# Optimization experiments

Measured on AMD Instinct MI355X. Metric: run time of the kernel, lower is better.

Reference implementation:

```python
import jax, jax.numpy as jnp
import numpy as np

N, E = 50000, 800000
IN, OUT = 128, 64
NEG_SLOPE = 0.2


def setup_inputs() -> dict:
    key = jax.random.key(0)
    ks = jax.random.split(key, 8)
    x = jax.random.normal(ks[0], (N, IN), dtype=jnp.float32)
    edge_index = jax.random.randint(ks[1], (2, E), 0, N, dtype=jnp.int64)
    s_in = 1.0 / np.sqrt(IN)
    s_out = 1.0 / np.sqrt(OUT)
    Wl = jax.random.normal(ks[2], (OUT, IN), dtype=jnp.float32) * s_in   # lin_l weight
    bl = jax.random.normal(ks[3], (OUT,), dtype=jnp.float32) * s_in     # lin_l bias
    Wr = jax.random.normal(ks[4], (OUT, IN), dtype=jnp.float32) * s_in  # lin_r weight
    br = jax.random.normal(ks[5], (OUT,), dtype=jnp.float32) * s_in     # lin_r bias
    att = jax.random.normal(ks[6], (OUT,), dtype=jnp.float32) * s_out   # attention vector a
    bias = jnp.zeros((OUT,), dtype=jnp.float32)                          # final output bias
    return dict(x=x, Wl=Wl, bl=bl, Wr=Wr, br=br, att=att, bias=bias, edge_index=edge_index)


def reference(x, Wl, bl, Wr, br, att, bias, edge_index):
    n = x.shape[0]
    loop = jnp.arange(n, dtype=edge_index.dtype)
    src = jnp.concatenate([edge_index[0], loop])  # add_self_loops=True
    dst = jnp.concatenate([edge_index[1], loop])
    xl = x @ Wl.T + bl  # [N, OUT] source transform (x_j)
    xr = x @ Wr.T + br  # [N, OUT] target transform (x_i)
    h = xl[src] + xr[dst]                              # [E+N, OUT]
    h = jnp.where(h > 0, h, NEG_SLOPE * h)             # LeakyReLU(0.2)
    e = h @ att                                        # [E+N] edge logits
    # segment softmax over destination nodes (every node has a self-loop)
    m = jax.ops.segment_max(e, dst, num_segments=n)
    ex = jnp.exp(e - m[dst])
    s = jax.ops.segment_sum(ex, dst, num_segments=n)
    alpha = ex / s[dst]
    out = jax.ops.segment_sum(alpha[:, None] * xl[src], dst, num_segments=n) + bias
    return jax.nn.relu(out)  # norm=Identity, dropout inactive at inference
```

## Files before the change

### kernel.cpp

```cpp
#include <hip/hip_runtime.h>
#include <hip/hip_bf16.h>

#define NEG_SLOPE 0.2f
#define CAP 5120
#define CHUNK 4096
#define LOG2E 1.4426950408889634f

typedef __attribute__((ext_vector_type(8))) short short8v;
typedef __attribute__((ext_vector_type(4))) short short4v;
typedef __attribute__((ext_vector_type(4))) float f32x4;

__device__ __forceinline__ short f2bf(float f) {
  __hip_bfloat16 b = __float2bfloat16(f);
  return *reinterpret_cast<short*>(&b);
}
__device__ __forceinline__ float bf2f(short s) {
  return __uint_as_float(((unsigned)(unsigned short)s) << 16);
}

__device__ __forceinline__ float row_reduce16(float p) {
  p += __int_as_float(__builtin_amdgcn_update_dpp(
      0, __float_as_int(p), 0xB1, 0xF, 0xF, true));
  p += __int_as_float(__builtin_amdgcn_update_dpp(
      0, __float_as_int(p), 0x4E, 0xF, 0xF, true));
  p += __int_as_float(__builtin_amdgcn_update_dpp(
      0, __float_as_int(p), 0x124, 0xF, 0xF, true));
  p += __int_as_float(__builtin_amdgcn_update_dpp(
      0, __float_as_int(p), 0x128, 0xF, 0xF, true));
  return p;
}

__global__ __launch_bounds__(256) void k_prep(
    const float* __restrict__ Wl, const float* __restrict__ Wr,
    const float* __restrict__ bl, const float* __restrict__ br,
    short* __restrict__ W2, float* __restrict__ biasc,
    int* __restrict__ bcur, int nbk) {
  int idx = blockIdx.x * 256 + threadIdx.x;
  if (idx < 128 * 128) {
    int j = idx >> 7, k = idx & 127;
    float v = (j < 64) ? Wl[j * 128 + k] : Wr[(j - 64) * 128 + k];
    W2[idx] = f2bf(v);
  } else {
    int z = idx - 128 * 128;
    if (z < nbk) bcur[z] = 0;
  }
  if (idx < 128) biasc[idx] = (idx < 64) ? bl[idx] : br[idx - 64];
}

__global__ __launch_bounds__(256) void k_tbf(
    const float* __restrict__ x, const short* __restrict__ W2,
    const float* __restrict__ biasc, const int* __restrict__ eidx,
    int* __restrict__ bcur, unsigned* __restrict__ pk,
    short* __restrict__ xlb, float* __restrict__ xr, int nN, int E_,
    int nbf) {
  __shared__ union {
    struct { int hist[256]; int base[256]; } bf;
    short xs[64 * 136];
  } u;
  const int t = threadIdx.x;

  if (blockIdx.x < nbf) {
    u.bf.hist[t] = 0;
    __syncthreads();
    const int e0 = blockIdx.x * CHUNK + t * 16;
    unsigned mypk[16];
    int myrank[16];
    const bool valid = (e0 < E_);
    if (valid) {
      const int4* ps = (const int4*)(eidx + e0);
      const int4* pd = (const int4*)(eidx + E_ + e0);
#pragma unroll
      for (int j = 0; j < 4; ++j) {
        int4 sv = ps[j];
        int4 dv = pd[j];
        int ss[4] = {sv.x, sv.y, sv.z, sv.w};
        int dd[4] = {dv.x, dv.y, dv.z, dv.w};
#pragma unroll
        for (int q = 0; q < 4; ++q) {
          unsigned p = ((unsigned)dd[q] << 16) | (unsigned)ss[q];
          mypk[j * 4 + q] = p;
          myrank[j * 4 + q] = atomicAdd(&u.bf.hist[dd[q] >> 8], 1);
        }
      }
    }
    __syncthreads();
    u.bf.base[t] = u.bf.hist[t] ? atomicAdd(&bcur[t], u.bf.hist[t]) : 0;
    __syncthreads();
    if (valid) {
#pragma unroll
      for (int j = 0; j < 16; ++j) {
        int b = mypk[j] >> 24;
        unsigned idx = (unsigned)(u.bf.base[b] + myrank[j]);
        if (idx < CAP) pk[(unsigned)b * CAP + idx] = mypk[j];
      }
    }
    return;
  }

  const int n0 = (blockIdx.x - nbf) * 64;
#pragma unroll
  for (int i = 0; i < 8; ++i) {
    int f = (i * 256 + t) * 4;
    int node = f >> 7, k = f & 127;
    int gn = min(n0 + node, nN - 1);
    float4 v = *(const float4*)(x + (size_t)gn * 128 + k);
    short4v s4;
    s4[0] = f2bf(v.x); s4[1] = f2bf(v.y); s4[2] = f2bf(v.z); s4[3] = f2bf(v.w);
    *(short4v*)(u.xs + node * 136 + k) = s4;
  }
  __syncthreads();

  const int w = t >> 6;
  const int lane = t & 63;
  const int r = lane & 15;
  const int kb = lane >> 4;

  short8v bfr[2][4];
#pragma unroll
  for (int c = 0; c < 2; ++c) {
    const short* bp = W2 + (size_t)((w * 2 + c) * 16 + r) * 128 + kb * 8;
#pragma unroll
    for (int kk = 0; kk < 4; ++kk) bfr[c][kk] = *(const short8v*)(bp + kk * 32);
  }

  f32x4 acc[4][2];
#pragma unroll
  for (int nt = 0; nt < 4; ++nt)
#pragma unroll
    for (int c = 0; c < 2; ++c) acc[nt][c] = (f32x4){0.f, 0.f, 0.f, 0.f};

#pragma unroll
  for (int nt = 0; nt < 4; ++nt) {
    short8v afr[4];
#pragma unroll
    for (int kk = 0; kk < 4; ++kk)
      afr[kk] =
          *(const short8v*)(u.xs + (nt * 16 + r) * 136 + kb * 8 + kk * 32);
#pragma unroll
    for (int kk = 0; kk < 4; ++kk) {
      acc[nt][0] =
          __builtin_amdgcn_mfma_f32_16x16x32_bf16(afr[kk], bfr[0][kk],
                                                  acc[nt][0], 0, 0, 0);
      acc[nt][1] =
          __builtin_amdgcn_mfma_f32_16x16x32_bf16(afr[kk], bfr[1][kk],
                                                  acc[nt][1], 0, 0, 0);
    }
  }

#pragma unroll
  for (int c = 0; c < 2; ++c) {
    const int ch = (w * 2 + c) * 16 + r;
    const float bv = biasc[ch];
#pragma unroll
    for (int nt = 0; nt < 4; ++nt) {
#pragma unroll
      for (int i = 0; i < 4; ++i) {
        int node = n0 + nt * 16 + kb * 4 + i;
        if (node < nN) {
          float v = acc[nt][c][i] + bv;
          if (ch < 64) xlb[(size_t)node * 64 + ch] = f2bf(v);
          else         xr[(size_t)node * 64 + (ch - 64)] = v;
        }
      }
    }
  }
}

__global__ __launch_bounds__(256) void k_nfill(
    const unsigned* __restrict__ pk, const int* __restrict__ bcur,
    int* __restrict__ rowlo, int* __restrict__ rowhi,
    unsigned short* __restrict__ csr, int nN) {
  __shared__ int hist[256];
  __shared__ int nbase[256];
  __shared__ int wsum[4];
  const int b = blockIdx.x;
  const int t = threadIdx.x;
  const int nb0 = b << 8;
  const int cnt = min(bcur[b], CAP);
  const unsigned gbase = (unsigned)b * CAP;
  hist[t] = 0;
  __syncthreads();
  for (int i = t; i < cnt; i += 256)
    atomicAdd(&hist[(pk[gbase + i] >> 16) & 255], 1);
  __syncthreads();
  const int lane = t & 63;
  const int wid = t >> 6;
  int v = hist[t];
  const int orig = v;
#pragma unroll
  for (int off = 1; off < 64; off <<= 1) {
    int uu = __shfl_up(v, off);
    if (lane >= off) v += uu;
  }
  if (lane == 63) wsum[wid] = v;
  __syncthreads();
  int add = 0;
  for (int ww = 0; ww < wid; ++ww) add += wsum[ww];
  const int excl = v - orig + add;
  nbase[t] = excl;
  if (nb0 + t < nN) {
    rowlo[nb0 + t] = (int)gbase + excl;
    rowhi[nb0 + t] = (int)gbase + excl + orig;
  }
  __syncthreads();
  hist[t] = 0;
  __syncthreads();
  for (int i = t; i < cnt; i += 256) {
    unsigned p = pk[gbase + i];
    int dl = (p >> 16) & 255;
    int slot = nbase[dl] + atomicAdd(&hist[dl], 1);
    csr[gbase + slot] = (unsigned short)(p & 0xFFFFu);
  }
}

__global__ __launch_bounds__(256) void k_node(
    const int* __restrict__ rowlo, const int* __restrict__ rowhi,
    const unsigned short* __restrict__ csr, const short* __restrict__ xlb,
    const float* __restrict__ xr, const float* __restrict__ att,
    const float* __restrict__ bias, float* __restrict__ out, int nN) {
  const int wid = (blockIdx.x * 256 + threadIdx.x) >> 6;
  if (wid >= nN) return;
  const int lane = threadIdx.x & 63;
  const int g = lane >> 4;
  const int r = lane & 15;
  const int d = wid;

  const float4 att4 = ((const float4*)att)[r];
  const float4 xr4 = *(const float4*)(xr + (size_t)d * 64 + r * 4);

  short4v sb = *(const short4v*)(xlb + (size_t)d * 64 + r * 4);
  float4 xls = make_float4(bf2f(sb[0]), bf2f(sb[1]), bf2f(sb[2]), bf2f(sb[3]));

  float hh, ps = 0.f;
  hh = xls.x + xr4.x; hh = fmaxf(hh, NEG_SLOPE * hh); ps = fmaf(hh, att4.x, ps);
  hh = xls.y + xr4.y; hh = fmaxf(hh, NEG_SLOPE * hh); ps = fmaf(hh, att4.y, ps);
  hh = xls.z + xr4.z; hh = fmaxf(hh, NEG_SLOPE * hh); ps = fmaf(hh, att4.z, ps);
  hh = xls.w + xr4.w; hh = fmaxf(hh, NEG_SLOPE * hh); ps = fmaf(hh, att4.w, ps);
  ps = row_reduce16(ps) * LOG2E;

  const bool g0 = (g == 0);
  float m = ps;
  float ssum = g0 ? 1.f : 0.f;
  float4 acc = g0 ? xls : make_float4(0.f, 0.f, 0.f, 0.f);

  const int lo = rowlo[d], hi = rowhi[d];
  const int nst = (hi - lo + 3) >> 2;

#define PROC(VREG, SIDX)                                                      \
  {                                                                           \
    const bool act = ((SIDX) < hi);                                           \
    float4 xlv = make_float4(bf2f(VREG[0]), bf2f(VREG[1]), bf2f(VREG[2]),     \
                             bf2f(VREG[3]));                                  \
    float p = 0.f;                                                            \
    hh = xlv.x + xr4.x; hh = fmaxf(hh, NEG_SLOPE * hh);                       \
    p = fmaf(hh, att4.x, p);                                                  \
    hh = xlv.y + xr4.y; hh = fmaxf(hh, NEG_SLOPE * hh);                       \
    p = fmaf(hh, att4.y, p);                                                  \
    hh = xlv.z + xr4.z; hh = fmaxf(hh, NEG_SLOPE * hh);                       \
    p = fmaf(hh, att4.z, p);                                                  \
    hh = xlv.w + xr4.w; hh = fmaxf(hh, NEG_SLOPE * hh);                       \
    p = fmaf(hh, att4.w, p);                                                  \
    p = row_reduce16(p);                                                      \
    const float pm = act ? p * LOG2E : -3.0e38f;                              \
    const float nm = fmaxf(m, pm);                                            \
    const float sc = exp2f(m - nm);                                           \
    const float w = exp2f(pm - nm);                                           \
    ssum = fmaf(ssum, sc, w);                                                 \
    acc.x = fmaf(acc.x, sc, w * xlv.x);                                       \
    acc.y = fmaf(acc.y, sc, w * xlv.y);                                       \
    acc.z = fmaf(acc.z, sc, w * xlv.z);                                       \
    acc.w = fmaf(acc.w, sc, w * xlv.w);                                       \
    m = nm;                                                                   \
  }

  int sA = lo + g, sB = sA + 4, sC = sA + 8, sD = sA + 12;
  short4v vA, vB, vC, vD;
  {
    int srcA = (sA < hi) ? (int)csr[sA] : d;
    vA = *(const short4v*)(xlb + (size_t)srcA * 64 + r * 4);
    int srcB = (sB < hi) ? (int)csr[sB] : d;
    vB = *(const short4v*)(xlb + (size_t)srcB * 64 + r * 4);
    int srcC = (sC < hi) ? (int)csr[sC] : d;
    vC = *(const short4v*)(xlb + (size_t)srcC * 64 + r * 4);
    int srcD = (sD < hi) ? (int)csr[sD] : d;
    vD = *(const short4v*)(xlb + (size_t)srcD * 64 + r * 4);
  }

  int tt = 0;
  for (; tt + 3 < nst; tt += 4) {
    PROC(vA, sA);
    if (tt + 4 < nst) {
      int sN = sA + 16;
      int srcN = (sN < hi) ? (int)csr[sN] : d;
      vA = *(const short4v*)(xlb + (size_t)srcN * 64 + r * 4);
    }
    PROC(vB, sB);
    if (tt + 5 < nst) {
      int sN = sB + 16;
      int srcN = (sN < hi) ? (int)csr[sN] : d;
      vB = *(const short4v*)(xlb + (size_t)srcN * 64 + r * 4);
    }
    PROC(vC, sC);
    if (tt + 6 < nst) {
      int sN = sC + 16;
      int srcN = (sN < hi) ? (int)csr[sN] : d;
      vC = *(const short4v*)(xlb + (size_t)srcN * 64 + r * 4);
    }
    PROC(vD, sD);
    if (tt + 7 < nst) {
      int sN = sD + 16;
      int srcN = (sN < hi) ? (int)csr[sN] : d;
      vD = *(const short4v*)(xlb + (size_t)srcN * 64 + r * 4);
    }
    sA += 16; sB += 16; sC += 16; sD += 16;
  }
  {
    const int rem = nst - tt;
    if (rem > 0) PROC(vA, sA);
    if (rem > 1) PROC(vB, sB);
    if (rem > 2) PROC(vC, sC);
  }
#undef PROC

#pragma unroll
  for (int off = 16; off <= 32; off <<= 1) {
    float mo = __shfl_xor(m, off);
    float so = __shfl_xor(ssum, off);
    float ax = __shfl_xor(acc.x, off);
    float ay = __shfl_xor(acc.y, off);
    float az = __shfl_xor(acc.z, off);
    float aw = __shfl_xor(acc.w, off);
    float nm = fmaxf(m, mo);
    float sa = exp2f(m - nm);
    float sb2 = exp2f(mo - nm);
    ssum = ssum * sa + so * sb2;
    acc.x = acc.x * sa + ax * sb2;
    acc.y = acc.y * sa + ay * sb2;
    acc.z = acc.z * sa + az * sb2;
    acc.w = acc.w * sa + aw * sb2;
    m = nm;
  }

  if (g == 0) {
    const float inv = 1.0f / ssum;
    const float4 b4 = ((const float4*)bias)[r];
    float4 o;
    o.x = fmaxf(fmaf(acc.x, inv, b4.x), 0.f);
    o.y = fmaxf(fmaf(acc.y, inv, b4.y), 0.f);
    o.z = fmaxf(fmaf(acc.z, inv, b4.z), 0.f);
    o.w = fmaxf(fmaf(acc.w, inv, b4.w), 0.f);
    *(float4*)(out + (size_t)d * 64 + r * 4) = o;
  }
}

extern "C" void kernel_launch(void* const* d_in, const int* in_sizes, int n_in,
                              void* d_out, int out_size, void* d_ws,
                              size_t ws_size, hipStream_t stream) {
  const float* x    = (const float*)d_in[0];
  const float* Wl   = (const float*)d_in[1];
  const float* bl   = (const float*)d_in[2];
  const float* Wr   = (const float*)d_in[3];
  const float* br   = (const float*)d_in[4];
  const float* att  = (const float*)d_in[5];
  const float* bias = (const float*)d_in[6];
  const int* eidx   = (const int*)d_in[7];
  float* out = (float*)d_out;

  const int N = in_sizes[0] / 128;
  const int E = in_sizes[7] / 2;
  const int NB = (N + 255) >> 8;
  const int nbf = (E + CHUNK - 1) / CHUNK;
  const int ntr = (N + 63) / 64;

  short* xlb   = (short*)d_ws;
  float* xr    = (float*)(xlb + (size_t)N * 64);
  unsigned* pk = (unsigned*)(xr + (size_t)N * 64);
  unsigned short* csr = (unsigned short*)(pk + (size_t)NB * CAP);
  short* W2    = (short*)(csr + (size_t)NB * CAP);
  float* biasc = (float*)(W2 + 128 * 128);
  int* bcur    = (int*)(biasc + 128);
  int* rowlo   = bcur + NB;
  int* rowhi   = rowlo + N;

  k_prep<<<(128 * 128 + NB + 255) / 256, 256, 0, stream>>>(
      Wl, Wr, bl, br, W2, biasc, bcur, NB);
  k_tbf<<<nbf + ntr, 256, 0, stream>>>(x, W2, biasc, eidx, bcur, pk, xlb, xr,
                                       N, E, nbf);
  k_nfill<<<NB, 256, 0, stream>>>(pk, bcur, rowlo, rowhi, csr, N);
  k_node<<<(N + 3) / 4, 256, 0, stream>>>(rowlo, rowhi, csr, xlb, xr, att,
                                          bias, out, N);
}
```

Before: 82.06 us.

## Split each wave into eight 8-lane edge groups and skip redundant softmax rescales

Result: faster. 78.09 us (-4.8%).

```diff
diff --git a/kernel.cpp b/kernel.cpp
--- a/kernel.cpp
+++ b/kernel.cpp
@@ -18,15 +18,13 @@
   return __uint_as_float(((unsigned)(unsigned short)s) << 16);
 }
 
-__device__ __forceinline__ float row_reduce16(float p) {
+__device__ __forceinline__ float row_reduce8(float p) {
   p += __int_as_float(__builtin_amdgcn_update_dpp(
       0, __float_as_int(p), 0xB1, 0xF, 0xF, true));
   p += __int_as_float(__builtin_amdgcn_update_dpp(
       0, __float_as_int(p), 0x4E, 0xF, 0xF, true));
   p += __int_as_float(__builtin_amdgcn_update_dpp(
-      0, __float_as_int(p), 0x124, 0xF, 0xF, true));
-  p += __int_as_float(__builtin_amdgcn_update_dpp(
-      0, __float_as_int(p), 0x128, 0xF, 0xF, true));
+      0, __float_as_int(p), 0x141, 0xF, 0xF, true));
   return p;
 }
 
@@ -221,135 +219,156 @@
   const int wid = (blockIdx.x * 256 + threadIdx.x) >> 6;
   if (wid >= nN) return;
   const int lane = threadIdx.x & 63;
-  const int g = lane >> 4;
-  const int r = lane & 15;
+  const int g = lane >> 3;
+  const int r = lane & 7;
   const int d = wid;
 
-  const float4 att4 = ((const float4*)att)[r];
-  const float4 xr4 = *(const float4*)(xr + (size_t)d * 64 + r * 4);
-
-  short4v sb = *(const short4v*)(xlb + (size_t)d * 64 + r * 4);
-  float4 xls = make_float4(bf2f(sb[0]), bf2f(sb[1]), bf2f(sb[2]), bf2f(sb[3]));
+  const float4 atA = *(const float4*)(att + r * 8);
+  const float4 atB = *(const float4*)(att + r * 8 + 4);
+  const float4 xrA = *(const float4*)(xr + (size_t)d * 64 + r * 8);
+  const float4 xrB = *(const float4*)(xr + (size_t)d * 64 + r * 8 + 4);
+
+  short8v sv = *(const short8v*)(xlb + (size_t)d * 64 + r * 8);
+  const float s0 = bf2f(sv[0]), s1 = bf2f(sv[1]), s2 = bf2f(sv[2]),
+              s3 = bf2f(sv[3]), s4 = bf2f(sv[4]), s5 = bf2f(sv[5]),
+              s6 = bf2f(sv[6]), s7 = bf2f(sv[7]);
 
   float hh, ps = 0.f;
-  hh = xls.x + xr4.x; hh = fmaxf(hh, NEG_SLOPE * hh); ps = fmaf(hh, att4.x, ps);
-  hh = xls.y + xr4.y; hh = fmaxf(hh, NEG_SLOPE * hh); ps = fmaf(hh, att4.y, ps);
-  hh = xls.z + xr4.z; hh = fmaxf(hh, NEG_SLOPE * hh); ps = fmaf(hh, att4.z, ps);
-  hh = xls.w + xr4.w; hh = fmaxf(hh, NEG_SLOPE * hh); ps = fmaf(hh, att4.w, ps);
-  ps = row_reduce16(ps) * LOG2E;
+  hh = s0 + xrA.x; hh = fmaxf(hh, NEG_SLOPE * hh); ps = fmaf(hh, atA.x, ps);
+  hh = s1 + xrA.y; hh = fmaxf(hh, NEG_SLOPE * hh); ps = fmaf(hh, atA.y, ps);
+  hh = s2 + xrA.z; hh = fmaxf(hh, NEG_SLOPE * hh); ps = fmaf(hh, atA.z, ps);
+  hh = s3 + xrA.w; hh = fmaxf(hh, NEG_SLOPE * hh); ps = fmaf(hh, atA.w, ps);
+  hh = s4 + xrB.x; hh = fmaxf(hh, NEG_SLOPE * hh); ps = fmaf(hh, atB.x, ps);
+  hh = s5 + xrB.y; hh = fmaxf(hh, NEG_SLOPE * hh); ps = fmaf(hh, atB.y, ps);
+  hh = s6 + xrB.z; hh = fmaxf(hh, NEG_SLOPE * hh); ps = fmaf(hh, atB.z, ps);
+  hh = s7 + xrB.w; hh = fmaxf(hh, NEG_SLOPE * hh); ps = fmaf(hh, atB.w, ps);
+  ps = row_reduce8(ps) * LOG2E;
 
   const bool g0 = (g == 0);
   float m = ps;
   float ssum = g0 ? 1.f : 0.f;
-  float4 acc = g0 ? xls : make_float4(0.f, 0.f, 0.f, 0.f);
+  float4 accA = g0 ? make_float4(s0, s1, s2, s3) : make_float4(0, 0, 0, 0);
+  float4 accB = g0 ? make_float4(s4, s5, s6, s7) : make_float4(0, 0, 0, 0);
 
   const int lo = rowlo[d], hi = rowhi[d];
-  const int nst = (hi - lo + 3) >> 2;
+  const int nst = (hi - lo + 7) >> 3;
 
 #define PROC(VREG, SIDX)                                                      \
   {                                                                           \
     const bool act = ((SIDX) < hi);                                           \
-    float4 xlv = make_float4(bf2f(VREG[0]), bf2f(VREG[1]), bf2f(VREG[2]),     \
-                             bf2f(VREG[3]));                                  \
+    const float f0 = bf2f(VREG[0]), f1 = bf2f(VREG[1]), f2 = bf2f(VREG[2]),   \
+                f3 = bf2f(VREG[3]), f4 = bf2f(VREG[4]), f5 = bf2f(VREG[5]),   \
+                f6 = bf2f(VREG[6]), f7 = bf2f(VREG[7]);                       \
     float p = 0.f;                                                            \
-    hh = xlv.x + xr4.x; hh = fmaxf(hh, NEG_SLOPE * hh);                       \
-    p = fmaf(hh, att4.x, p);                                                  \
-    hh = xlv.y + xr4.y; hh = fmaxf(hh, NEG_SLOPE * hh);                       \
-    p = fmaf(hh, att4.y, p);                                                  \
-    hh = xlv.z + xr4.z; hh = fmaxf(hh, NEG_SLOPE * hh);                       \
-    p = fmaf(hh, att4.z, p);                                                  \
-    hh = xlv.w + xr4.w; hh = fmaxf(hh, NEG_SLOPE * hh);                       \
-    p = fmaf(hh, att4.w, p);                                                  \
-    p = row_reduce16(p);                                                      \
+    hh = f0 + xrA.x; hh = fmaxf(hh, NEG_SLOPE * hh); p = fmaf(hh, atA.x, p);  \
+    hh = f1 + xrA.y; hh = fmaxf(hh, NEG_SLOPE * hh); p = fmaf(hh, atA.y, p);  \
+    hh = f2 + xrA.z; hh = fmaxf(hh, NEG_SLOPE * hh); p = fmaf(hh, atA.z, p);  \
+    hh = f3 + xrA.w; hh = fmaxf(hh, NEG_SLOPE * hh); p = fmaf(hh, atA.w, p);  \
+    hh = f4 + xrB.x; hh = fmaxf(hh, NEG_SLOPE * hh); p = fmaf(hh, atB.x, p);  \
+    hh = f5 + xrB.y; hh = fmaxf(hh, NEG_SLOPE * hh); p = fmaf(hh, atB.y, p);  \
+    hh = f6 + xrB.z; hh = fmaxf(hh, NEG_SLOPE * hh); p = fmaf(hh, atB.z, p);  \
+    hh = f7 + xrB.w; hh = fmaxf(hh, NEG_SLOPE * hh); p = fmaf(hh, atB.w, p);  \
+    p = row_reduce8(p);                                                       \
     const float pm = act ? p * LOG2E : -3.0e38f;                              \
-    const float nm = fmaxf(m, pm);                                            \
-    const float sc = exp2f(m - nm);                                           \
-    const float w = exp2f(pm - nm);                                           \
-    ssum = fmaf(ssum, sc, w);                                                 \
-    acc.x = fmaf(acc.x, sc, w * xlv.x);                                       \
-    acc.y = fmaf(acc.y, sc, w * xlv.y);                                       \
-    acc.z = fmaf(acc.z, sc, w * xlv.z);                                       \
-    acc.w = fmaf(acc.w, sc, w * xlv.w);                                       \
-    m = nm;                                                                   \
-  }
-
-  int sA = lo + g, sB = sA + 4, sC = sA + 8, sD = sA + 12;
-  short4v vA, vB, vC, vD;
+    if (__any(pm > m)) {                  \
+      const float nm = fmaxf(m, pm);                                          \
+      const float sc = exp2f(m - nm);                                         \
+      const float w = exp2f(pm - nm);                                         \
+      ssum = fmaf(ssum, sc, w);                                               \
+      accA.x = fmaf(accA.x, sc, w * f0);                                      \
+      accA.y = fmaf(accA.y, sc, w * f1);                                      \
+      accA.z = fmaf(accA.z, sc, w * f2);                                      \
+      accA.w = fmaf(accA.w, sc, w * f3);                                      \
+      accB.x = fmaf(accB.x, sc, w * f4);                                      \
+      accB.y = fmaf(accB.y, sc, w * f5);                                      \
+      accB.z = fmaf(accB.z, sc, w * f6);                                      \
+      accB.w = fmaf(accB.w, sc, w * f7);                                      \
+      m = nm;                                                                 \
+    } else {                   \
+      const float w = exp2f(pm - m);                                          \
+      ssum += w;                                                              \
+      accA.x = fmaf(w, f0, accA.x);                                           \
+      accA.y = fmaf(w, f1, accA.y);                                           \
+      accA.z = fmaf(w, f2, accA.z);                                           \
+      accA.w = fmaf(w, f3, accA.w);                                           \
+      accB.x = fmaf(w, f4, accB.x);                                           \
+      accB.y = fmaf(w, f5, accB.y);                                           \
+      accB.z = fmaf(w, f6, accB.z);                                           \
+      accB.w = fmaf(w, f7, accB.w);                                           \
+    }                                                                         \
+  }
+
+  int sA = lo + g, sB = sA + 8;
+  short8v vA, vB;
   {
     int srcA = (sA < hi) ? (int)csr[sA] : d;
-    vA = *(const short4v*)(xlb + (size_t)srcA * 64 + r * 4);
+    vA = *(const short8v*)(xlb + (size_t)srcA * 64 + r * 8);
     int srcB = (sB < hi) ? (int)csr[sB] : d;
-    vB = *(const short4v*)(xlb + (size_t)srcB * 64 + r * 4);
-    int srcC = (sC < hi) ? (int)csr[sC] : d;
-    vC = *(const short4v*)(xlb + (size_t)srcC * 64 + r * 4);
-    int srcD = (sD < hi) ? (int)csr[sD] : d;
-    vD = *(const short4v*)(xlb + (size_t)srcD * 64 + r * 4);
+    vB = *(const short8v*)(xlb + (size_t)srcB * 64 + r * 8);
   }
 
   int tt = 0;
-  for (; tt + 3 < nst; tt += 4) {
+  for (; tt + 1 < nst; tt += 2) {
     PROC(vA, sA);
-    if (tt + 4 < nst) {
+    if (tt + 2 < nst) {
       int sN = sA + 16;
       int srcN = (sN < hi) ? (int)csr[sN] : d;
-      vA = *(const short4v*)(xlb + (size_t)srcN * 64 + r * 4);
+      vA = *(const short8v*)(xlb + (size_t)srcN * 64 + r * 8);
     }
     PROC(vB, sB);
-    if (tt + 5 < nst) {
+    if (tt + 3 < nst) {
       int sN = sB + 16;
       int srcN = (sN < hi) ? (int)csr[sN] : d;
-      vB = *(const short4v*)(xlb + (size_t)srcN * 64 + r * 4);
-    }
-    PROC(vC, sC);
-    if (tt + 6 < nst) {
-      int sN = sC + 16;
-      int srcN = (sN < hi) ? (int)csr[sN] : d;
-      vC = *(const short4v*)(xlb + (size_t)srcN * 64 + r * 4);
-    }
-    PROC(vD, sD);
-    if (tt + 7 < nst) {
-      int sN = sD + 16;
-      int srcN = (sN < hi) ? (int)csr[sN] : d;
-      vD = *(const short4v*)(xlb + (size_t)srcN * 64 + r * 4);
-    }
-    sA += 16; sB += 16; sC += 16; sD += 16;
-  }
-  {
-    const int rem = nst - tt;
-    if (rem > 0) PROC(vA, sA);
-    if (rem > 1) PROC(vB, sB);
-    if (rem > 2) PROC(vC, sC);
-  }
+      vB = *(const short8v*)(xlb + (size_t)srcN * 64 + r * 8);
+    }
+    sA += 16;
+    sB += 16;
+  }
+  if (tt < nst) PROC(vA, sA);
 #undef PROC
 
 #pragma unroll
-  for (int off = 16; off <= 32; off <<= 1) {
+  for (int off = 8; off <= 32; off <<= 1) {
     float mo = __shfl_xor(m, off);
     float so = __shfl_xor(ssum, off);
-    float ax = __shfl_xor(acc.x, off);
-    float ay = __shfl_xor(acc.y, off);
-    float az = __shfl_xor(acc.z, off);
-    float aw = __shfl_xor(acc.w, off);
+    float a0 = __shfl_xor(accA.x, off);
+    float a1 = __shfl_xor(accA.y, off);
+    float a2 = __shfl_xor(accA.z, off);
+    float a3 = __shfl_xor(accA.w, off);
+    float a4 = __shfl_xor(accB.x, off);
+    float a5 = __shfl_xor(accB.y, off);
+    float a6 = __shfl_xor(accB.z, off);
+    float a7 = __shfl_xor(accB.w, off);
     float nm = fmaxf(m, mo);
     float sa = exp2f(m - nm);
     float sb2 = exp2f(mo - nm);
     ssum = ssum * sa + so * sb2;
-    acc.x = acc.x * sa + ax * sb2;
-    acc.y = acc.y * sa + ay * sb2;
-    acc.z = acc.z * sa + az * sb2;
-    acc.w = acc.w * sa + aw * sb2;
+    accA.x = accA.x * sa + a0 * sb2;
+    accA.y = accA.y * sa + a1 * sb2;
+    accA.z = accA.z * sa + a2 * sb2;
+    accA.w = accA.w * sa + a3 * sb2;
+    accB.x = accB.x * sa + a4 * sb2;
+    accB.y = accB.y * sa + a5 * sb2;
+    accB.z = accB.z * sa + a6 * sb2;
+    accB.w = accB.w * sa + a7 * sb2;
     m = nm;
   }
 
   if (g == 0) {
     const float inv = 1.0f / ssum;
-    const float4 b4 = ((const float4*)bias)[r];
-    float4 o;
-    o.x = fmaxf(fmaf(acc.x, inv, b4.x), 0.f);
-    o.y = fmaxf(fmaf(acc.y, inv, b4.y), 0.f);
-    o.z = fmaxf(fmaf(acc.z, inv, b4.z), 0.f);
-    o.w = fmaxf(fmaf(acc.w, inv, b4.w), 0.f);
-    *(float4*)(out + (size_t)d * 64 + r * 4) = o;
+    const float4 bA = *(const float4*)(bias + r * 8);
+    const float4 bB = *(const float4*)(bias + r * 8 + 4);
+    float4 oA, oB;
+    oA.x = fmaxf(fmaf(accA.x, inv, bA.x), 0.f);
+    oA.y = fmaxf(fmaf(accA.y, inv, bA.y), 0.f);
+    oA.z = fmaxf(fmaf(accA.z, inv, bA.z), 0.f);
+    oA.w = fmaxf(fmaf(accA.w, inv, bA.w), 0.f);
+    oB.x = fmaxf(fmaf(accB.x, inv, bB.x), 0.f);
+    oB.y = fmaxf(fmaf(accB.y, inv, bB.y), 0.f);
+    oB.z = fmaxf(fmaf(accB.z, inv, bB.z), 0.f);
+    oB.w = fmaxf(fmaf(accB.w, inv, bB.w), 0.f);
+    *(float4*)(out + (size_t)d * 64 + r * 8) = oA;
+    *(float4*)(out + (size_t)d * 64 + r * 8 + 4) = oB;
   }
 }
 
```
